# Performance work log

Hardware: AMD Instinct MI355X
Metric: run time of the kernel (lower is better)

The kernel has to match this reference:

```python
import jax, jax.numpy as jnp
import numpy as np

_BIG = 1e4  # kornia uses 1e4 as the 'infinity' for masked-out kernel positions


def _windows(img, pad_val):
    """Return the 9 shifted 3x3 neighborhoods of img, stacked on axis 0.
    img: [B,C,H,W] -> [9,B,C,H,W]. Border padded with pad_val so padded
    pixels never win the min (erosion) / max (dilation), matching kornia.
    """
    B, C, H, W = img.shape
    p = jnp.pad(img, ((0, 0), (0, 0), (1, 1), (1, 1)), constant_values=pad_val)
    return jnp.stack([p[..., i:i + H, j:j + W]
                      for i in range(3) for j in range(3)], axis=0)


def _erosion(img, mask):
    w = _windows(img, _BIG)
    return jnp.min(jnp.where(mask, w, _BIG), axis=0)


def _dilation(img, mask):
    w = _windows(img, -_BIG)
    return jnp.max(jnp.where(mask, w, -_BIG), axis=0)


def setup_inputs() -> dict:
    key = jax.random.key(0)
    img = jax.random.uniform(key, (8, 3, 1024, 1024), dtype=jnp.float32)
    # kernel0: symmetric 3x3 cross structuring element
    kernel = jnp.array([[0, 1, 0], [1, 1, 1], [0, 1, 0]], dtype=jnp.int32)
    return {"img": img, "kernel": kernel}


def reference(img, kernel):
    # morphological opening = erosion followed by dilation, same structuring element
    mask = (kernel.reshape(9, 1, 1, 1, 1) == 1)
    eroded = _erosion(img, mask)
    opened = _dilation(eroded, mask)
    return opened
```

## Files before the change

### kernel.cpp

```cpp
#include <hip/hip_runtime.h>

#define BIGV 1e4f

constexpr int RH = 8;
constexpr int TY = 4;
constexpr int PX = 8;

typedef float nf4 __attribute__((ext_vector_type(4)));

struct Raw { float4 m0, m1; float2 L, R; };
struct Ero { float e[10]; };

__device__ __forceinline__ float min3f(float a, float b, float c) { return fminf(fminf(a, b), c); }
__device__ __forceinline__ float max3f(float a, float b, float c) { return fmaxf(fmaxf(a, b), c); }

__device__ __forceinline__ float rv(const Raw& r, int i) {
    switch (i) {
        case 0:  return r.L.x;  case 1:  return r.L.y;
        case 2:  return r.m0.x; case 3:  return r.m0.y;
        case 4:  return r.m0.z; case 5:  return r.m0.w;
        case 6:  return r.m1.x; case 7:  return r.m1.y;
        case 8:  return r.m1.z; case 9:  return r.m1.w;
        case 10: return r.R.x;  default: return r.R.y;
    }
}

__device__ __forceinline__ Raw load_raw(const float* __restrict__ img, int y, int x,
                                        int H, int W) {
    Raw r;
    if (y >= 0 && y < H) {
        const float* q = img + (size_t)y * W;
        r.m0 = *(const float4*)(q + x);
        r.m1 = *(const float4*)(q + x + 4);
        r.L = make_float2(BIGV, BIGV);
        r.R = make_float2(BIGV, BIGV);
        if (x > 0)      r.L = *(const float2*)(q + x - 2);
        if (x + PX < W) r.R = *(const float2*)(q + x + PX);
    } else {
        r.m0 = make_float4(BIGV, BIGV, BIGV, BIGV);
        r.m1 = r.m0;
        r.L = make_float2(BIGV, BIGV);
        r.R = r.L;
    }
    return r;
}

__device__ __forceinline__ Ero erode_cross(const Raw& a, const Raw& b, const Raw& c,
                                           int y, int H, int x, int W) {
    Ero e;
    if (y >= 0 && y < H) {
#pragma unroll
        for (int j = 0; j < 10; ++j) {
            float v = min3f(rv(a, j + 1), rv(b, j + 1), rv(c, j + 1));
            e.e[j] = min3f(v, rv(b, j), rv(b, j + 2));
        }
        if (x == 0)      e.e[0] = -BIGV;
        if (x + PX >= W) e.e[9] = -BIGV;
    } else {
#pragma unroll
        for (int j = 0; j < 10; ++j) e.e[j] = -BIGV;
    }
    return e;
}

__device__ __forceinline__ void dilate_cross(const Ero& t, const Ero& m, const Ero& b,
                                             nf4& o0, nf4& o1) {
    float o[PX];
#pragma unroll
    for (int j = 0; j < PX; ++j)
        o[j] = max3f(max3f(t.e[j + 1], m.e[j + 1], b.e[j + 1]), m.e[j], m.e[j + 2]);
    o0 = (nf4){o[0], o[1], o[2], o[3]};
    o1 = (nf4){o[4], o[5], o[6], o[7]};
}

__device__ __forceinline__ Ero erode_gen(const Raw& a, const Raw& b, const Raw& c,
                                         const bool* m, int y, int H, int x, int W) {
    Ero e;
    if (y >= 0 && y < H) {
#pragma unroll
        for (int j = 0; j < 10; ++j) {
            float acc = BIGV;
#pragma unroll
            for (int k = 0; k < 9; ++k) {
                const int di = k / 3, dj = k % 3;
                const Raw& rr = (di == 0) ? a : ((di == 1) ? b : c);
                acc = fminf(acc, m[k] ? rv(rr, j + dj) : BIGV);
            }
            e.e[j] = acc;
        }
        if (x == 0)      e.e[0] = -BIGV;
        if (x + PX >= W) e.e[9] = -BIGV;
    } else {
#pragma unroll
        for (int j = 0; j < 10; ++j) e.e[j] = -BIGV;
    }
    return e;
}

__device__ __forceinline__ void dilate_gen(const Ero& t, const Ero& md, const Ero& b,
                                           const bool* m, nf4& o0, nf4& o1) {
    float o[PX];
#pragma unroll
    for (int j = 0; j < PX; ++j) {
        float acc = -BIGV;
#pragma unroll
        for (int k = 0; k < 9; ++k) {
            const int di = k / 3, dj = k % 3;
            const Ero& ee = (di == 0) ? t : ((di == 1) ? md : b);
            acc = fmaxf(acc, m[k] ? ee.e[j + dj] : -BIGV);
        }
        o[j] = acc;
    }
    o0 = (nf4){o[0], o[1], o[2], o[3]};
    o1 = (nf4){o[4], o[5], o[6], o[7]};
}

template <bool CROSS>
__device__ __forceinline__ void run(const float* __restrict__ img, float* __restrict__ out,
                                    const bool* m, int x, int y0, int H, int W) {
    Raw r0 = load_raw(img, y0 - 2, x, H, W);
    Raw r1 = load_raw(img, y0 - 1, x, H, W);
    Raw r2 = load_raw(img, y0,     x, H, W);
    Raw r3 = load_raw(img, y0 + 1, x, H, W);
    Raw pf = load_raw(img, y0 + 2, x, H, W);

    Ero E0 = CROSS ? erode_cross(r0, r1, r2, y0 - 1, H, x, W)
                   : erode_gen(r0, r1, r2, m, y0 - 1, H, x, W);
    Ero E1 = CROSS ? erode_cross(r1, r2, r3, y0, H, x, W)
                   : erode_gen(r1, r2, r3, m, y0, H, x, W);
    Raw A = r2, B = r3;

#pragma unroll
    for (int i = 0; i < RH; ++i) {
        const int y = y0 + i;
        Raw nf = pf;
        if (i < RH - 1)
            nf = load_raw(img, y + 3, x, H, W);
        Ero E2 = CROSS ? erode_cross(A, B, pf, y + 1, H, x, W)
                       : erode_gen(A, B, pf, m, y + 1, H, x, W);
        nf4 o0, o1;
        if (CROSS) dilate_cross(E0, E1, E2, o0, o1);
        else       dilate_gen(E0, E1, E2, m, o0, o1);
        float* po = out + (size_t)y * W + x;
        __builtin_nontemporal_store(o0, (nf4*)po);
        __builtin_nontemporal_store(o1, (nf4*)(po + 4));
        A = B; B = pf; pf = nf;
        E0 = E1; E1 = E2;
    }
}

__global__ __launch_bounds__(256) void opening_kernel(
    const float* __restrict__ img, const int* __restrict__ kern,
    float* __restrict__ out, int H, int W)
{
    const int lx = threadIdx.x & 63;
    const int ty = threadIdx.x >> 6;
    const int x  = blockIdx.x * (64 * PX) + lx * PX;
    const int y0 = (blockIdx.y * TY + ty) * RH;
    const size_t pbase = (size_t)blockIdx.z * H * W;

    bool m[9];
#pragma unroll
    for (int k = 0; k < 9; ++k) m[k] = (kern[k] == 1);

    const bool cross = m[1] && m[3] && m[4] && m[5] && m[7] &&
                       !m[0] && !m[2] && !m[6] && !m[8];

    if (cross) run<true >(img + pbase, out + pbase, m, x, y0, H, W);
    else       run<false>(img + pbase, out + pbase, m, x, y0, H, W);
}

extern "C" void kernel_launch(void* const* d_in, const int* in_sizes, int n_in,
                              void* d_out, int out_size, void* d_ws, size_t ws_size,
                              hipStream_t stream) {
    const float* img  = (const float*)d_in[0];
    const int*   kern = (const int*)d_in[1];
    float*       out  = (float*)d_out;

    const int H = 1024, W = 1024;
    const int planes = in_sizes[0] / (H * W);

    dim3 block(256);
    dim3 grid(W / (64 * PX), H / (TY * RH), planes);
    opening_kernel<<<grid, block, 0, stream>>>(img, kern, out, H, W);
}
```

Before: 187.8 us.

## Batch row prefetch in groups of four and double rows per thread

```diff
diff --git a/kernel.cpp b/kernel.cpp
--- a/kernel.cpp
+++ b/kernel.cpp
@@ -2,11 +2,11 @@
 
 #define BIGV 1e4f
 
-constexpr int RH = 8;
+constexpr int PX = 8;
+constexpr int D  = 4;
+constexpr int PH = 4;
+constexpr int RH = D * PH;
 constexpr int TY = 4;
-constexpr int PX = 8;
-
-typedef float nf4 __attribute__((ext_vector_type(4)));
 
 struct Raw { float4 m0, m1; float2 L, R; };
 struct Ero { float e[10]; };
@@ -64,13 +64,13 @@
 }
 
 __device__ __forceinline__ void dilate_cross(const Ero& t, const Ero& m, const Ero& b,
-                                             nf4& o0, nf4& o1) {
+                                             float4& o0, float4& o1) {
     float o[PX];
 #pragma unroll
     for (int j = 0; j < PX; ++j)
         o[j] = max3f(max3f(t.e[j + 1], m.e[j + 1], b.e[j + 1]), m.e[j], m.e[j + 2]);
-    o0 = (nf4){o[0], o[1], o[2], o[3]};
-    o1 = (nf4){o[4], o[5], o[6], o[7]};
+    o0 = make_float4(o[0], o[1], o[2], o[3]);
+    o1 = make_float4(o[4], o[5], o[6], o[7]);
 }
 
 __device__ __forceinline__ Ero erode_gen(const Raw& a, const Raw& b, const Raw& c,
@@ -98,7 +98,7 @@
 }
 
 __device__ __forceinline__ void dilate_gen(const Ero& t, const Ero& md, const Ero& b,
-                                           const bool* m, nf4& o0, nf4& o1) {
+                                           const bool* m, float4& o0, float4& o1) {
     float o[PX];
 #pragma unroll
     for (int j = 0; j < PX; ++j) {
@@ -111,45 +111,56 @@
         }
         o[j] = acc;
     }
-    o0 = (nf4){o[0], o[1], o[2], o[3]};
-    o1 = (nf4){o[4], o[5], o[6], o[7]};
+    o0 = make_float4(o[0], o[1], o[2], o[3]);
+    o1 = make_float4(o[4], o[5], o[6], o[7]);
 }
 
 template <bool CROSS>
 __device__ __forceinline__ void run(const float* __restrict__ img, float* __restrict__ out,
                                     const bool* m, int x, int y0, int H, int W) {
-    Raw r0 = load_raw(img, y0 - 2, x, H, W);
-    Raw r1 = load_raw(img, y0 - 1, x, H, W);
-    Raw r2 = load_raw(img, y0,     x, H, W);
-    Raw r3 = load_raw(img, y0 + 1, x, H, W);
-    Raw pf = load_raw(img, y0 + 2, x, H, W);
+    Raw p0 = load_raw(img, y0 - 2, x, H, W);
+    Raw p1 = load_raw(img, y0 - 1, x, H, W);
+    Raw A  = load_raw(img, y0,     x, H, W);
+    Raw B  = load_raw(img, y0 + 1, x, H, W);
+    Raw rc[D];
+#pragma unroll
+    for (int j = 0; j < D; ++j) rc[j] = load_raw(img, y0 + 2 + j, x, H, W);
 
-    Ero E0 = CROSS ? erode_cross(r0, r1, r2, y0 - 1, H, x, W)
-                   : erode_gen(r0, r1, r2, m, y0 - 1, H, x, W);
-    Ero E1 = CROSS ? erode_cross(r1, r2, r3, y0, H, x, W)
-                   : erode_gen(r1, r2, r3, m, y0, H, x, W);
-    Raw A = r2, B = r3;
+    Ero E0 = CROSS ? erode_cross(p0, p1, A, y0 - 1, H, x, W)
+                   : erode_gen(p0, p1, A, m, y0 - 1, H, x, W);
+    Ero E1 = CROSS ? erode_cross(p1, A, B, y0, H, x, W)
+                   : erode_gen(p1, A, B, m, y0, H, x, W);
 
 #pragma unroll
-    for (int i = 0; i < RH; ++i) {
-        const int y = y0 + i;
-        Raw nf = pf;
-        if (i < RH - 1)
-            nf = load_raw(img, y + 3, x, H, W);
-        Ero E2 = CROSS ? erode_cross(A, B, pf, y + 1, H, x, W)
-                       : erode_gen(A, B, pf, m, y + 1, H, x, W);
-        nf4 o0, o1;
-        if (CROSS) dilate_cross(E0, E1, E2, o0, o1);
-        else       dilate_gen(E0, E1, E2, m, o0, o1);
-        float* po = out + (size_t)y * W + x;
-        __builtin_nontemporal_store(o0, (nf4*)po);
-        __builtin_nontemporal_store(o1, (nf4*)(po + 4));
-        A = B; B = pf; pf = nf;
-        E0 = E1; E1 = E2;
+    for (int p = 0; p < PH; ++p) {
+        const int yb = y0 + p * D;
+        Raw rn[D];
+        if (p < PH - 1) {
+#pragma unroll
+            for (int j = 0; j < D; ++j) rn[j] = load_raw(img, yb + D + 2 + j, x, H, W);
+        }
+#pragma unroll
+        for (int i = 0; i < D; ++i) {
+            const int y = yb + i;
+            Ero E2 = CROSS ? erode_cross(A, B, rc[i], y + 1, H, x, W)
+                           : erode_gen(A, B, rc[i], m, y + 1, H, x, W);
+            float4 o0, o1;
+            if (CROSS) dilate_cross(E0, E1, E2, o0, o1);
+            else       dilate_gen(E0, E1, E2, m, o0, o1);
+            float* po = out + (size_t)y * W + x;
+            *(float4*)po       = o0;
+            *((float4*)po + 1) = o1;
+            A = B; B = rc[i];
+            E0 = E1; E1 = E2;
+        }
+        if (p < PH - 1) {
+#pragma unroll
+            for (int j = 0; j < D; ++j) rc[j] = rn[j];
+        }
     }
 }
 
-__global__ __launch_bounds__(256) void opening_kernel(
+__global__ __launch_bounds__(256, 3) void opening_kernel(
     const float* __restrict__ img, const int* __restrict__ kern,
     float* __restrict__ out, int H, int W)
 {
```

Result: no change. 190.7 us (+1.5%).
